# Optimization experiments

Measured on AMD Instinct MI355X. Metric: run time of the kernel, lower is better.

Reference implementation:

```python
import jax, jax.numpy as jnp
import numpy as np

ALPHA = 0.1
K_STEPS = 10


def _with_self_loops(edge_index, n):
    loops = jnp.arange(n, dtype=edge_index.dtype)
    src = jnp.concatenate([edge_index[0], loops])
    dst = jnp.concatenate([edge_index[1], loops])
    return src, dst


def _gcn_norm(src, dst, n, dtype):
    # symmetric normalization deg^{-1/2}[src] * deg^{-1/2}[dst], deg over in-edges (incl. self loops)
    deg = jax.ops.segment_sum(jnp.ones(dst.shape[0], dtype=dtype), dst, num_segments=n)
    dinv = jnp.where(deg > 0, jax.lax.rsqrt(deg), jnp.zeros_like(deg))
    return dinv[src] * dinv[dst]


def _propagate(h, src, dst, norm, n):
    # gather -> scale -> scatter-add (A_hat @ h)
    msg = h[src] * norm[:, None]            # [E, d]
    return jax.ops.segment_sum(msg, dst, num_segments=n)


def setup_inputs() -> dict:
    key = jax.random.key(0)
    ks = jax.random.split(key, 8)
    N, E, D, H, C = 100000, 3200000, 256, 256, 40
    s = 1.0 / np.sqrt(D)
    return {
        "x": jax.random.normal(ks[0], (N, D), dtype=jnp.float32),
        "edge_index": jax.random.randint(ks[1], (2, E), 0, N, dtype=jnp.int64),
        "w1": jax.random.normal(ks[2], (D, H), dtype=jnp.float32) * s,
        "b1": jnp.zeros((H,), dtype=jnp.float32),
        "w2": jax.random.normal(ks[3], (H, H), dtype=jnp.float32) * s,
        "b2": jnp.zeros((H,), dtype=jnp.float32),
        "w3": jax.random.normal(ks[4], (H, H), dtype=jnp.float32) * s,
        "b3": jnp.zeros((H,), dtype=jnp.float32),
        "fc_w": jax.random.normal(ks[5], (H, C), dtype=jnp.float32) * s,
        "fc_b": jnp.zeros((C,), dtype=jnp.float32),
    }


def reference(x, edge_index, w1, b1, w2, b2, w3, b3, fc_w, fc_b):
    n = x.shape[0]
    src, dst = _with_self_loops(edge_index, n)
    norm = _gcn_norm(src, dst, n, x.dtype)

    def gcn_conv(h, w, b):
        h = h @ w                             # linear transform first (PyG GCNConv)
        return _propagate(h, src, dst, norm, n) + b

    h = jax.nn.relu(gcn_conv(x, w1, b1))
    h = jax.nn.relu(gcn_conv(h, w2, b2))
    h = jax.nn.relu(gcn_conv(h, w3, b3))      # convx with layer=3 has one extra GCNConv

    # APPNP: K steps of h <- (1-alpha) * A_hat h + alpha * h0
    h0 = h
    def step(h, _):
        h = (1.0 - ALPHA) * _propagate(h, src, dst, norm, n) + ALPHA * h0
        return h, None
    h, _ = jax.lax.scan(step, h, None, length=K_STEPS)

    logits = h @ fc_w + fc_b
    return jax.nn.log_softmax(logits, axis=1)
```

## Files before the change

kernel.cpp:

```cpp
#include <hip/hip_runtime.h>
#include <math.h>


constexpr int D  = 256;
constexpr int C  = 40;
constexpr int ZP = 64;

typedef _Float16 h2v    __attribute__((ext_vector_type(2)));
typedef _Float16 h4     __attribute__((ext_vector_type(4)));
typedef _Float16 half8v __attribute__((ext_vector_type(8)));
typedef float    f32x4  __attribute__((ext_vector_type(4)));

struct __align__(8) EdgeCV { int c; float v; };


__global__ void k_init_cnt(int* __restrict__ cnt, int N) {
    int i = blockIdx.x * blockDim.x + threadIdx.x;
    if (i < N) cnt[i] = 1;
}

__global__ void k_count(const int* __restrict__ dst, int* __restrict__ cnt, int E) {
    int e = blockIdx.x * blockDim.x + threadIdx.x;
    if (e < E) atomicAdd(&cnt[dst[e]], 1);
}

__global__ void k_alloc(const int* __restrict__ cnt, int* __restrict__ startA,
                        int* __restrict__ cursor, int N) {
    int i = blockIdx.x * blockDim.x + threadIdx.x;
    if (i < N) startA[i] = atomicAdd(cursor, cnt[i]);
}

__global__ void k_selfinit(const int* __restrict__ cnt, const int* __restrict__ startA,
                           float* __restrict__ dinv, EdgeCV* __restrict__ edges,
                           int* __restrict__ fill, int N) {
    int i = blockIdx.x * blockDim.x + threadIdx.x;
    if (i < N) {
        float dv = rsqrtf((float)cnt[i]);
        dinv[i] = dv;
        EdgeCV e; e.c = i; e.v = dv * dv;
        edges[startA[i]] = e;
        fill[i] = 1;
    }
}

__global__ void k_fill_edges(const int* __restrict__ src, const int* __restrict__ dst,
                             const int* __restrict__ startA, const float* __restrict__ dinv,
                             EdgeCV* __restrict__ edges, int* __restrict__ fill, int E) {
    int e = blockIdx.x * blockDim.x + threadIdx.x;
    if (e < E) {
        int s = src[e], d = dst[e];
        int slot = atomicAdd(&fill[d], 1);
        EdgeCV ev; ev.c = s; ev.v = dinv[s] * dinv[d];
        edges[startA[d] + slot] = ev;
    }
}


__global__ void k_transW(const float* __restrict__ W0, const float* __restrict__ W1,
                         const float* __restrict__ W2, _Float16* __restrict__ Wt) {
    int n = blockIdx.x;
    int w = blockIdx.y;
    int k = threadIdx.x;
    const float* W = (w == 0) ? W0 : (w == 1) ? W1 : W2;
    Wt[(size_t)w * 65536 + n * 256 + k] = (_Float16)W[k * 256 + n];
}


template <typename TIN>
__global__ __launch_bounds__(256, 1) void k_gemm_mfma(const TIN* __restrict__ A,
                                                      const _Float16* __restrict__ Wt,
                                                      _Float16* __restrict__ Cout, int M) {
    __shared__ _Float16 wlds[256][72];
    const int tid  = threadIdx.x;
    const int lane = tid & 63;
    const int wave = tid >> 6;
    const int l15  = lane & 15;
    const int lk8  = (lane >> 4) * 8;
    const int rowbase = blockIdx.x * 128 + wave * 32;

    half8v a[2][8];
    #pragma unroll
    for (int mt = 0; mt < 2; ++mt) {
        int row = rowbase + mt * 16 + l15;
        bool ok = row < M;
        const TIN* ap = A + (size_t)(ok ? row : 0) * D;
        #pragma unroll
        for (int kk = 0; kk < 8; ++kk) {
            half8v v;
            if constexpr (sizeof(TIN) == 2) {
                v = *(const half8v*)(ap + kk * 32 + lk8);
            } else {
                float4 f0 = *(const float4*)(ap + kk * 32 + lk8);
                float4 f1 = *(const float4*)(ap + kk * 32 + lk8 + 4);
                v[0] = (_Float16)f0.x; v[1] = (_Float16)f0.y;
                v[2] = (_Float16)f0.z; v[3] = (_Float16)f0.w;
                v[4] = (_Float16)f1.x; v[5] = (_Float16)f1.y;
                v[6] = (_Float16)f1.z; v[7] = (_Float16)f1.w;
            }
            if (!ok) {
                half8v zz = {0, 0, 0, 0, 0, 0, 0, 0};
                v = zz;
            }
            a[mt][kk] = v;
        }
    }

    f32x4 acc[2][16] = {};

    #pragma unroll
    for (int s = 0; s < 4; ++s) {
        {
            const half8v* srcp = (const half8v*)(Wt + (size_t)tid * D + s * 64);
            #pragma unroll
            for (int cc = 0; cc < 8; ++cc)
                *(half8v*)(&wlds[tid][cc * 8]) = srcp[cc];
        }
        __syncthreads();
        #pragma unroll
        for (int kf = 0; kf < 2; ++kf) {
            const int kk = s * 2 + kf;
            #pragma unroll
            for (int nt = 0; nt < 16; ++nt) {
                half8v b = *(const half8v*)(&wlds[nt * 16 + l15][kf * 32 + lk8]);
                acc[0][nt] = __builtin_amdgcn_mfma_f32_16x16x32_f16(a[0][kk], b, acc[0][nt], 0, 0, 0);
                acc[1][nt] = __builtin_amdgcn_mfma_f32_16x16x32_f16(a[1][kk], b, acc[1][nt], 0, 0, 0);
            }
        }
        __syncthreads();
    }

    const int r0 = (lane >> 4) * 4;
    #pragma unroll
    for (int mt = 0; mt < 2; ++mt) {
        #pragma unroll
        for (int r = 0; r < 4; ++r) {
            int row = rowbase + mt * 16 + r0 + r;
            if (row < M) {
                _Float16* crow = Cout + (size_t)row * D;
                #pragma unroll
                for (int nt = 0; nt < 16; ++nt)
                    crow[nt * 16 + l15] = (_Float16)acc[mt][nt][r];
            }
        }
    }
}


__global__ __launch_bounds__(256) void k_spmm_relu(const _Float16* __restrict__ h,
                                                   const int* __restrict__ startA,
                                                   const int* __restrict__ cnt,
                                                   const EdgeCV* __restrict__ edges,
                                                   const float* __restrict__ bias,
                                                   _Float16* __restrict__ out, int N) {
    int gid  = (int)((blockIdx.x * 256u + threadIdx.x) >> 6);
    int lane = threadIdx.x & 63;
    if (gid >= N) return;
    int start = startA[gid], end = start + cnt[gid];
    const h4* hp = (const h4*)h;
    float4 s0 = make_float4(0.f, 0.f, 0.f, 0.f);
    float4 s1 = make_float4(0.f, 0.f, 0.f, 0.f);
    float4 s2 = make_float4(0.f, 0.f, 0.f, 0.f);
    float4 s3 = make_float4(0.f, 0.f, 0.f, 0.f);
    int e = start;
    for (; e + 3 < end; e += 4) {
        EdgeCV c0 = edges[e],     c1 = edges[e + 1];
        EdgeCV c2 = edges[e + 2], c3 = edges[e + 3];
        h4 x0 = hp[(size_t)c0.c * 64 + lane];
        h4 x1 = hp[(size_t)c1.c * 64 + lane];
        h4 x2 = hp[(size_t)c2.c * 64 + lane];
        h4 x3 = hp[(size_t)c3.c * 64 + lane];
        s0.x += c0.v * (float)x0[0]; s0.y += c0.v * (float)x0[1];
        s0.z += c0.v * (float)x0[2]; s0.w += c0.v * (float)x0[3];
        s1.x += c1.v * (float)x1[0]; s1.y += c1.v * (float)x1[1];
        s1.z += c1.v * (float)x1[2]; s1.w += c1.v * (float)x1[3];
        s2.x += c2.v * (float)x2[0]; s2.y += c2.v * (float)x2[1];
        s2.z += c2.v * (float)x2[2]; s2.w += c2.v * (float)x2[3];
        s3.x += c3.v * (float)x3[0]; s3.y += c3.v * (float)x3[1];
        s3.z += c3.v * (float)x3[2]; s3.w += c3.v * (float)x3[3];
    }
    for (; e < end; ++e) {
        EdgeCV c0 = edges[e];
        h4 x0 = hp[(size_t)c0.c * 64 + lane];
        s0.x += c0.v * (float)x0[0]; s0.y += c0.v * (float)x0[1];
        s0.z += c0.v * (float)x0[2]; s0.w += c0.v * (float)x0[3];
    }
    float4 acc = make_float4(s0.x + s1.x + s2.x + s3.x,
                             s0.y + s1.y + s2.y + s3.y,
                             s0.z + s1.z + s2.z + s3.z,
                             s0.w + s1.w + s2.w + s3.w);
    float4 b = ((const float4*)bias)[lane];
    h4 o;
    o[0] = (_Float16)fmaxf(acc.x + b.x, 0.f);
    o[1] = (_Float16)fmaxf(acc.y + b.y, 0.f);
    o[2] = (_Float16)fmaxf(acc.z + b.z, 0.f);
    o[3] = (_Float16)fmaxf(acc.w + b.w, 0.f);
    ((h4*)out)[(size_t)gid * 64 + lane] = o;
}


__global__ __launch_bounds__(256) void k_z0(const _Float16* __restrict__ h,
                                            const float* __restrict__ fcw,
                                            _Float16* __restrict__ z0, int N) {
    __shared__ float ws[D * C];
    for (int i = threadIdx.x; i < D * C; i += 256) ws[i] = fcw[i];
    __syncthreads();
    int row = blockIdx.x * 256 + threadIdx.x;
    if (row >= N) return;
    float acc[C] = {};
    const half8v* hr = (const half8v*)(h + (size_t)row * D);
    for (int kq = 0; kq < 32; ++kq) {
        half8v v = hr[kq];
        #pragma unroll
        for (int j = 0; j < 8; ++j) {
            float hv = (float)v[j];
            #pragma unroll
            for (int c = 0; c < C; ++c) acc[c] += hv * ws[(kq * 8 + j) * C + c];
        }
    }
    h2v* zr = (h2v*)(z0 + (size_t)row * ZP);
    #pragma unroll
    for (int c = 0; c < 20; ++c) {
        h2v o; o[0] = (_Float16)acc[2 * c]; o[1] = (_Float16)acc[2 * c + 1];
        zr[c] = o;
    }
    h2v zz = {(_Float16)0.f, (_Float16)0.f};
    #pragma unroll
    for (int c = 20; c < 32; ++c) zr[c] = zz;
}


__global__ __launch_bounds__(256) void k_spmm40(const _Float16* __restrict__ z,
                                                const int* __restrict__ startA,
                                                const int* __restrict__ cnt,
                                                const EdgeCV* __restrict__ edges,
                                                const _Float16* __restrict__ z0,
                                                _Float16* __restrict__ out, int N) {
    int wid  = (int)((blockIdx.x * 256u + threadIdx.x) >> 6);
    int lane = threadIdx.x & 63;
    int p    = lane >> 5;
    int l5   = lane & 31;
    int row  = wid * 2 + p;
    if (row >= N) return;
    int start = startA[row], end = start + cnt[row];
    const h2v* zp = (const h2v*)z;
    float ax0 = 0.f, ay0 = 0.f, ax1 = 0.f, ay1 = 0.f;
    float ax2 = 0.f, ay2 = 0.f, ax3 = 0.f, ay3 = 0.f;
    int e = start;
    for (; e + 3 < end; e += 4) {
        EdgeCV c0 = edges[e],     c1 = edges[e + 1];
        EdgeCV c2 = edges[e + 2], c3 = edges[e + 3];
        h2v x0 = zp[(size_t)c0.c * 32 + l5];
        h2v x1 = zp[(size_t)c1.c * 32 + l5];
        h2v x2 = zp[(size_t)c2.c * 32 + l5];
        h2v x3 = zp[(size_t)c3.c * 32 + l5];
        ax0 += c0.v * (float)x0[0]; ay0 += c0.v * (float)x0[1];
        ax1 += c1.v * (float)x1[0]; ay1 += c1.v * (float)x1[1];
        ax2 += c2.v * (float)x2[0]; ay2 += c2.v * (float)x2[1];
        ax3 += c3.v * (float)x3[0]; ay3 += c3.v * (float)x3[1];
    }
    for (; e < end; ++e) {
        EdgeCV c0 = edges[e];
        h2v x0 = zp[(size_t)c0.c * 32 + l5];
        ax0 += c0.v * (float)x0[0]; ay0 += c0.v * (float)x0[1];
    }
    float ax = ax0 + ax1 + ax2 + ax3;
    float ay = ay0 + ay1 + ay2 + ay3;
    h2v zz = ((const h2v*)z0)[(size_t)row * 32 + l5];
    ax = 0.9f * ax + 0.1f * (float)zz[0];
    ay = 0.9f * ay + 0.1f * (float)zz[1];
    h2v o; o[0] = (_Float16)ax; o[1] = (_Float16)ay;
    ((h2v*)out)[(size_t)row * 32 + l5] = o;
}


__global__ __launch_bounds__(256) void k_logsm(const _Float16* __restrict__ z,
                                               const float* __restrict__ fcb,
                                               float* __restrict__ out, int N) {
    __shared__ float bs[C];
    for (int i = threadIdx.x; i < C; i += 256) bs[i] = fcb[i];
    __syncthreads();
    int row = blockIdx.x * 256 + threadIdx.x;
    if (row >= N) return;
    float v[C];
    const h2v* zr = (const h2v*)(z + (size_t)row * ZP);
    #pragma unroll
    for (int c = 0; c < 20; ++c) {
        h2v t = zr[c];
        v[2 * c]     = (float)t[0] + bs[2 * c];
        v[2 * c + 1] = (float)t[1] + bs[2 * c + 1];
    }
    float m = v[0];
    #pragma unroll
    for (int c = 1; c < C; ++c) m = fmaxf(m, v[c]);
    float s = 0.f;
    #pragma unroll
    for (int c = 0; c < C; ++c) s += expf(v[c] - m);
    float lse = logf(s) + m;
    float* orow = out + (size_t)row * C;
    #pragma unroll
    for (int c = 0; c < C; ++c) orow[c] = v[c] - lse;
}


extern "C" void kernel_launch(void* const* d_in, const int* in_sizes, int n_in,
                              void* d_out, int out_size, void* d_ws, size_t ws_size,
                              hipStream_t stream) {
    const float* x   = (const float*)d_in[0];
    const int*   ei  = (const int*)d_in[1];
    const float* w1  = (const float*)d_in[2];
    const float* b1  = (const float*)d_in[3];
    const float* w2  = (const float*)d_in[4];
    const float* b2  = (const float*)d_in[5];
    const float* w3  = (const float*)d_in[6];
    const float* b3  = (const float*)d_in[7];
    const float* fcw = (const float*)d_in[8];
    const float* fcb = (const float*)d_in[9];
    float* out = (float*)d_out;

    const int N = in_sizes[0] / D;
    const int E = in_sizes[1] / 2;
    const int* srcArr = ei;
    const int* dstArr = ei + E;

    char* wsp = (char*)d_ws;
    size_t off = 0;
    auto take = [&](size_t bytes) -> void* {
        void* p = wsp + off;
        off = (off + bytes + 255) & ~(size_t)255;
        return p;
    };
    int*       cnt    = (int*)take((size_t)N * 4);
    int*       startA = (int*)take((size_t)N * 4);
    int*       fill   = (int*)take((size_t)N * 4);
    int*       cursor = (int*)take(256);
    float*     dinv   = (float*)take((size_t)N * 4);
    EdgeCV*    edges  = (EdgeCV*)take((size_t)(E + N) * 8);
    _Float16*  bufA   = (_Float16*)take((size_t)N * D * 2);
    _Float16*  bufB   = (_Float16*)take((size_t)N * D * 2);
    _Float16*  bufC   = (_Float16*)take((size_t)N * D * 2);
    _Float16*  Wt     = (_Float16*)take((size_t)3 * D * D * 2);
    _Float16*  z0w    = (_Float16*)take((size_t)N * ZP * 2);
    _Float16*  zA     = (_Float16*)take((size_t)N * ZP * 2);
    _Float16*  zB     = (_Float16*)take((size_t)N * ZP * 2);
    (void)ws_size;

    dim3 b256(256);
    int gN = (N + 255) / 256;
    int gE = (E + 255) / 256;

    hipMemsetAsync(cursor, 0, 4, stream);
    k_init_cnt<<<gN, b256, 0, stream>>>(cnt, N);
    k_count<<<gE, b256, 0, stream>>>(dstArr, cnt, E);
    k_alloc<<<gN, b256, 0, stream>>>(cnt, startA, cursor, N);
    k_selfinit<<<gN, b256, 0, stream>>>(cnt, startA, dinv, edges, fill, N);
    k_fill_edges<<<gE, b256, 0, stream>>>(srcArr, dstArr, startA, dinv, edges, fill, E);

    dim3 tg(256, 3);
    k_transW<<<tg, b256, 0, stream>>>(w1, w2, w3, Wt);

    dim3 gg((N + 127) / 128);
    int spBlocks  = (N + 3) / 4;
    int sp40Blocks = (N + 7) / 8;

    k_gemm_mfma<float><<<gg, b256, 0, stream>>>(x, Wt, bufA, N);
    k_spmm_relu<<<spBlocks, b256, 0, stream>>>(bufA, startA, cnt, edges, b1, bufB, N);
    k_gemm_mfma<_Float16><<<gg, b256, 0, stream>>>(bufB, Wt + 65536, bufA, N);
    k_spmm_relu<<<spBlocks, b256, 0, stream>>>(bufA, startA, cnt, edges, b2, bufB, N);
    k_gemm_mfma<_Float16><<<gg, b256, 0, stream>>>(bufB, Wt + 131072, bufA, N);
    k_spmm_relu<<<spBlocks, b256, 0, stream>>>(bufA, startA, cnt, edges, b3, bufC, N);

    k_z0<<<gN, b256, 0, stream>>>(bufC, fcw, z0w, N);

    const _Float16* zc = z0w;
    _Float16* zn = zA;
    for (int it = 0; it < 10; ++it) {
        k_spmm40<<<sp40Blocks, b256, 0, stream>>>(zc, startA, cnt, edges, z0w, zn, N);
        zc = zn;
        zn = (zn == zA) ? zB : zA;
    }

    k_logsm<<<gN, b256, 0, stream>>>(zc, fcb, out, N);
}
```

Before: 2.093 ms.

## Slice first-layer features into column panels and simplify CSR build

The first GEMM now writes its output in four 64-column slices, and a new sliced SpMM processes one slice per grid-y. The aim is to shrink the gather working set per pass so it fits better in cache. The CSR build is merged into fewer kernels: per-edge slots are recorded during counting, so the fill kernel needs no second atomic, and cnt now excludes the self loop. The APPNP SpMM loop is unrolled to 8 edges for more memory-level parallelism. Only layer 1 uses the sliced path; layers 2 and 3 keep the old one, and the new slot array costs E ints of extra memory traffic.

```diff
diff --git a/kernel.cpp b/kernel.cpp
--- a/kernel.cpp
+++ b/kernel.cpp
@@ -14,44 +14,35 @@
 struct __align__(8) EdgeCV { int c; float v; };
 
 
-__global__ void k_init_cnt(int* __restrict__ cnt, int N) {
-    int i = blockIdx.x * blockDim.x + threadIdx.x;
-    if (i < N) cnt[i] = 1;
-}
-
-__global__ void k_count(const int* __restrict__ dst, int* __restrict__ cnt, int E) {
+__global__ void k_count(const int* __restrict__ dst, int* __restrict__ cnt,
+                        int* __restrict__ eslot, int E) {
     int e = blockIdx.x * blockDim.x + threadIdx.x;
-    if (e < E) atomicAdd(&cnt[dst[e]], 1);
-}
-
-__global__ void k_alloc(const int* __restrict__ cnt, int* __restrict__ startA,
-                        int* __restrict__ cursor, int N) {
-    int i = blockIdx.x * blockDim.x + threadIdx.x;
-    if (i < N) startA[i] = atomicAdd(cursor, cnt[i]);
-}
-
-__global__ void k_selfinit(const int* __restrict__ cnt, const int* __restrict__ startA,
-                           float* __restrict__ dinv, EdgeCV* __restrict__ edges,
-                           int* __restrict__ fill, int N) {
+    if (e < E) eslot[e] = atomicAdd(&cnt[dst[e]], 1);
+}
+
+__global__ void k_alloc_self(const int* __restrict__ cnt, int* __restrict__ startA,
+                             int* __restrict__ cursor, float* __restrict__ dinv,
+                             EdgeCV* __restrict__ edges, int N) {
     int i = blockIdx.x * blockDim.x + threadIdx.x;
     if (i < N) {
-        float dv = rsqrtf((float)cnt[i]);
+        int c = cnt[i];
+        int s = atomicAdd(cursor, c + 1);
+        startA[i] = s;
+        float dv = rsqrtf((float)(c + 1));
         dinv[i] = dv;
-        EdgeCV e; e.c = i; e.v = dv * dv;
-        edges[startA[i]] = e;
-        fill[i] = 1;
-    }
-}
-
-__global__ void k_fill_edges(const int* __restrict__ src, const int* __restrict__ dst,
-                             const int* __restrict__ startA, const float* __restrict__ dinv,
-                             EdgeCV* __restrict__ edges, int* __restrict__ fill, int E) {
+        EdgeCV ev; ev.c = i; ev.v = dv * dv;
+        edges[s + c] = ev;
+    }
+}
+
+__global__ void k_fill(const int* __restrict__ src, const int* __restrict__ dst,
+                       const int* __restrict__ startA, const int* __restrict__ eslot,
+                       const float* __restrict__ dinv, EdgeCV* __restrict__ edges, int E) {
     int e = blockIdx.x * blockDim.x + threadIdx.x;
     if (e < E) {
         int s = src[e], d = dst[e];
-        int slot = atomicAdd(&fill[d], 1);
         EdgeCV ev; ev.c = s; ev.v = dinv[s] * dinv[d];
-        edges[startA[d] + slot] = ev;
+        edges[startA[d] + eslot[e]] = ev;
     }
 }
 
@@ -66,7 +57,7 @@
 }
 
 
-template <typename TIN>
+template <typename TIN, bool SLICED>
 __global__ __launch_bounds__(256, 1) void k_gemm_mfma(const TIN* __restrict__ A,
                                                       const _Float16* __restrict__ Wt,
                                                       _Float16* __restrict__ Cout, int M) {
@@ -77,6 +68,7 @@
     const int l15  = lane & 15;
     const int lk8  = (lane >> 4) * 8;
     const int rowbase = blockIdx.x * 128 + wave * 32;
+    const size_t sliceN = (size_t)M * 64;
 
     half8v a[2][8];
     #pragma unroll
@@ -136,13 +128,58 @@
         for (int r = 0; r < 4; ++r) {
             int row = rowbase + mt * 16 + r0 + r;
             if (row < M) {
-                _Float16* crow = Cout + (size_t)row * D;
-                #pragma unroll
-                for (int nt = 0; nt < 16; ++nt)
-                    crow[nt * 16 + l15] = (_Float16)acc[mt][nt][r];
+                if constexpr (SLICED) {
+                    #pragma unroll
+                    for (int nt = 0; nt < 16; ++nt) {
+                        int col = nt * 16 + l15;
+                        Cout[(size_t)(col >> 6) * sliceN + (size_t)row * 64 + (col & 63)]
+                            = (_Float16)acc[mt][nt][r];
+                    }
+                } else {
+                    _Float16* crow = Cout + (size_t)row * D;
+                    #pragma unroll
+                    for (int nt = 0; nt < 16; ++nt)
+                        crow[nt * 16 + l15] = (_Float16)acc[mt][nt][r];
+                }
             }
         }
     }
+}
+
+
+__global__ __launch_bounds__(256) void k_spmm_sliced(const _Float16* __restrict__ t,
+                                                     const int* __restrict__ startA,
+                                                     const int* __restrict__ cnt,
+                                                     const EdgeCV* __restrict__ edges,
+                                                     const float* __restrict__ bias,
+                                                     _Float16* __restrict__ out, int N) {
+    int gid   = (int)((blockIdx.x * 256u + threadIdx.x) >> 6);
+    int lane  = threadIdx.x & 63;
+    int slice = blockIdx.y;
+    if (gid >= N) return;
+    int start = startA[gid], end = start + cnt[gid] + 1;
+    const _Float16* ts = t + (size_t)slice * ((size_t)N * 64);
+    float a[8];
+    #pragma unroll
+    for (int i = 0; i < 8; ++i) a[i] = 0.f;
+    int e = start;
+    for (; e + 7 < end; e += 8) {
+        EdgeCV c[8];
+        float x[8];
+        #pragma unroll
+        for (int i = 0; i < 8; ++i) c[i] = edges[e + i];
+        #pragma unroll
+        for (int i = 0; i < 8; ++i) x[i] = (float)ts[(size_t)c[i].c * 64 + lane];
+        #pragma unroll
+        for (int i = 0; i < 8; ++i) a[i] += c[i].v * x[i];
+    }
+    for (; e < end; ++e) {
+        EdgeCV c0 = edges[e];
+        a[0] += c0.v * (float)ts[(size_t)c0.c * 64 + lane];
+    }
+    float acc = ((a[0] + a[1]) + (a[2] + a[3])) + ((a[4] + a[5]) + (a[6] + a[7]));
+    float b = bias[slice * 64 + lane];
+    out[(size_t)gid * D + slice * 64 + lane] = (_Float16)fmaxf(acc + b, 0.f);
 }
 
 
@@ -155,7 +192,7 @@
     int gid  = (int)((blockIdx.x * 256u + threadIdx.x) >> 6);
     int lane = threadIdx.x & 63;
     if (gid >= N) return;
-    int start = startA[gid], end = start + cnt[gid];
+    int start = startA[gid], end = start + cnt[gid] + 1;
     const h4* hp = (const h4*)h;
     float4 s0 = make_float4(0.f, 0.f, 0.f, 0.f);
     float4 s1 = make_float4(0.f, 0.f, 0.f, 0.f);
@@ -241,34 +278,36 @@
     int l5   = lane & 31;
     int row  = wid * 2 + p;
     if (row >= N) return;
-    int start = startA[row], end = start + cnt[row];
+    int start = startA[row], end = start + cnt[row] + 1;
     const h2v* zp = (const h2v*)z;
-    float ax0 = 0.f, ay0 = 0.f, ax1 = 0.f, ay1 = 0.f;
-    float ax2 = 0.f, ay2 = 0.f, ax3 = 0.f, ay3 = 0.f;
+    float ax[8], ay[8];
+    #pragma unroll
+    for (int i = 0; i < 8; ++i) { ax[i] = 0.f; ay[i] = 0.f; }
     int e = start;
-    for (; e + 3 < end; e += 4) {
-        EdgeCV c0 = edges[e],     c1 = edges[e + 1];
-        EdgeCV c2 = edges[e + 2], c3 = edges[e + 3];
-        h2v x0 = zp[(size_t)c0.c * 32 + l5];
-        h2v x1 = zp[(size_t)c1.c * 32 + l5];
-        h2v x2 = zp[(size_t)c2.c * 32 + l5];
-        h2v x3 = zp[(size_t)c3.c * 32 + l5];
-        ax0 += c0.v * (float)x0[0]; ay0 += c0.v * (float)x0[1];
-        ax1 += c1.v * (float)x1[0]; ay1 += c1.v * (float)x1[1];
-        ax2 += c2.v * (float)x2[0]; ay2 += c2.v * (float)x2[1];
-        ax3 += c3.v * (float)x3[0]; ay3 += c3.v * (float)x3[1];
+    for (; e + 7 < end; e += 8) {
+        EdgeCV c[8];
+        h2v x[8];
+        #pragma unroll
+        for (int i = 0; i < 8; ++i) c[i] = edges[e + i];
+        #pragma unroll
+        for (int i = 0; i < 8; ++i) x[i] = zp[(size_t)c[i].c * 32 + l5];
+        #pragma unroll
+        for (int i = 0; i < 8; ++i) {
+            ax[i] += c[i].v * (float)x[i][0];
+            ay[i] += c[i].v * (float)x[i][1];
+        }
     }
     for (; e < end; ++e) {
         EdgeCV c0 = edges[e];
         h2v x0 = zp[(size_t)c0.c * 32 + l5];
-        ax0 += c0.v * (float)x0[0]; ay0 += c0.v * (float)x0[1];
-    }
-    float ax = ax0 + ax1 + ax2 + ax3;
-    float ay = ay0 + ay1 + ay2 + ay3;
+        ax[0] += c0.v * (float)x0[0]; ay[0] += c0.v * (float)x0[1];
+    }
+    float axs = ((ax[0] + ax[1]) + (ax[2] + ax[3])) + ((ax[4] + ax[5]) + (ax[6] + ax[7]));
+    float ays = ((ay[0] + ay[1]) + (ay[2] + ay[3])) + ((ay[4] + ay[5]) + (ay[6] + ay[7]));
     h2v zz = ((const h2v*)z0)[(size_t)row * 32 + l5];
-    ax = 0.9f * ax + 0.1f * (float)zz[0];
-    ay = 0.9f * ay + 0.1f * (float)zz[1];
-    h2v o; o[0] = (_Float16)ax; o[1] = (_Float16)ay;
+    axs = 0.9f * axs + 0.1f * (float)zz[0];
+    ays = 0.9f * ays + 0.1f * (float)zz[1];
+    h2v o; o[0] = (_Float16)axs; o[1] = (_Float16)ays;
     ((h2v*)out)[(size_t)row * 32 + l5] = o;
 }
 
@@ -331,7 +370,7 @@
     };
     int*       cnt    = (int*)take((size_t)N * 4);
     int*       startA = (int*)take((size_t)N * 4);
-    int*       fill   = (int*)take((size_t)N * 4);
+    int*       eslot  = (int*)take((size_t)E * 4);
     int*       cursor = (int*)take(256);
     float*     dinv   = (float*)take((size_t)N * 4);
     EdgeCV*    edges  = (EdgeCV*)take((size_t)(E + N) * 8);
@@ -349,25 +388,25 @@
     int gE = (E + 255) / 256;
 
     hipMemsetAsync(cursor, 0, 4, stream);
-    k_init_cnt<<<gN, b256, 0, stream>>>(cnt, N);
-    k_count<<<gE, b256, 0, stream>>>(dstArr, cnt, E);
-    k_alloc<<<gN, b256, 0, stream>>>(cnt, startA, cursor, N);
-    k_selfinit<<<gN, b256, 0, stream>>>(cnt, startA, dinv, edges, fill, N);
-    k_fill_edges<<<gE, b256, 0, stream>>>(srcArr, dstArr, startA, dinv, edges, fill, E);
+    hipMemsetAsync(cnt, 0, (size_t)N * 4, stream);
+    k_count<<<gE, b256, 0, stream>>>(dstArr, cnt, eslot, E);
+    k_alloc_self<<<gN, b256, 0, stream>>>(cnt, startA, cursor, dinv, edges, N);
+    k_fill<<<gE, b256, 0, stream>>>(srcArr, dstArr, startA, eslot, dinv, edges, E);
 
     dim3 tg(256, 3);
     k_transW<<<tg, b256, 0, stream>>>(w1, w2, w3, Wt);
 
     dim3 gg((N + 127) / 128);
-    int spBlocks  = (N + 3) / 4;
+    int spBlocks   = (N + 3) / 4;
     int sp40Blocks = (N + 7) / 8;
-
-    k_gemm_mfma<float><<<gg, b256, 0, stream>>>(x, Wt, bufA, N);
-    k_spmm_relu<<<spBlocks, b256, 0, stream>>>(bufA, startA, cnt, edges, b1, bufB, N);
-    k_gemm_mfma<_Float16><<<gg, b256, 0, stream>>>(bufB, Wt + 65536, bufA, N);
-    k_spmm_relu<<<spBlocks, b256, 0, stream>>>(bufA, startA, cnt, edges, b2, bufB, N);
-    k_gemm_mfma<_Float16><<<gg, b256, 0, stream>>>(bufB, Wt + 131072, bufA, N);
-    k_spmm_relu<<<spBlocks, b256, 0, stream>>>(bufA, startA, cnt, edges, b3, bufC, N);
+    dim3 slicedGrid((N + 3) / 4, 4);
+
+    k_gemm_mfma<float, true><<<gg, b256, 0, stream>>>(x, Wt, bufB, N);
+    k_spmm_sliced<<<slicedGrid, b256, 0, stream>>>(bufB, startA, cnt, edges, b1, bufA, N);
+    k_gemm_mfma<_Float16, false><<<gg, b256, 0, stream>>>(bufA, Wt + 65536, bufB, N);
+    k_spmm_relu<<<spBlocks, b256, 0, stream>>>(bufB, startA, cnt, edges, b2, bufA, N);
+    k_gemm_mfma<_Float16, false><<<gg, b256, 0, stream>>>(bufA, Wt + 131072, bufB, N);
+    k_spmm_relu<<<spBlocks, b256, 0, stream>>>(bufB, startA, cnt, edges, b3, bufC, N);
 
     k_z0<<<gN, b256, 0, stream>>>(bufC, fcw, z0w, N);
 
```

Result: no change. 2.115 ms (+1.0%).
